# Performance work log

Measured on AMD Instinct MI355X. Metric: run time of the kernel, lower is better.

## Reference

```python
import jax, jax.numpy as jnp
import numpy as np
import math

BLK_NUM, BLK_SIZE = 128, 8
DIM, N_HEADS, N_KV_HEADS = 1024, 16, 4
HEAD_DIM = DIM // N_HEADS            # 64
HIDDEN = 64 * ((DIM + 63) // 64)     # 1024 (FeedForward hidden_dim)
BATCH = 4
SEQ = BLK_NUM * BLK_SIZE             # 1024
EPS = 1e-6
ROPE_THETA = 10000.0


def setup_inputs() -> dict:
    key = jax.random.key(0)
    ks = jax.random.split(key, 12)
    std = 1.0 / math.sqrt(DIM)
    f32 = jnp.float32
    inp = {
        "x":   jax.random.normal(ks[0], (BATCH, SEQ, DIM), f32),
        "vec": jax.random.normal(ks[1], (BATCH, BLK_NUM, DIM), f32),
        "wq": jax.random.normal(ks[2], (N_HEADS * HEAD_DIM, DIM), f32) * std,
        "wk": jax.random.normal(ks[3], (N_KV_HEADS * HEAD_DIM, DIM), f32) * std,
        "wv": jax.random.normal(ks[4], (N_KV_HEADS * HEAD_DIM, DIM), f32) * std,
        "wo": jax.random.normal(ks[5], (DIM, N_HEADS * HEAD_DIM), f32) * std,
        "w1": jax.random.normal(ks[6], (HIDDEN, DIM), f32) * std,
        "w2": jax.random.normal(ks[7], (DIM, HIDDEN), f32) * std,
        "w3": jax.random.normal(ks[8], (HIDDEN, DIM), f32) * std,
        "mod_attn_w": jax.random.normal(ks[9], (3 * DIM, DIM), f32) * std,
        "mod_attn_b": jnp.zeros((3 * DIM,), f32),
        "mod_ffn_w":  jax.random.normal(ks[10], (3 * DIM, DIM), f32) * std,
        "mod_ffn_b":  jnp.zeros((3 * DIM,), f32),
        "norm1_w": jnp.ones((DIM,), f32),
        "norm2_w": jnp.ones((DIM,), f32),
    }
    # rotary tables (equivalent to llama-style precompute_freqs_cis, theta=rope_scaling)
    inv_freq = 1.0 / (ROPE_THETA ** (jnp.arange(0, HEAD_DIM, 2, dtype=f32) / HEAD_DIM))
    angles = jnp.outer(jnp.arange(SEQ, dtype=f32), inv_freq)  # (SEQ, HEAD_DIM//2)
    inp["freqs_cos"] = jnp.cos(angles)
    inp["freqs_sin"] = jnp.sin(angles)
    return inp


def _rmsnorm(x, w):
    return x * jax.lax.rsqrt(jnp.mean(x * x, axis=-1, keepdims=True) + EPS) * w


def _rope(x, cos, sin):
    # x: (B, L, H, Dh); pairs are adjacent dims, matching view_as_complex on (..., Dh//2, 2)
    x1, x2 = x[..., 0::2], x[..., 1::2]
    c, s = cos[None, :, None, :], sin[None, :, None, :]
    return jnp.stack([x1 * c - x2 * s, x1 * s + x2 * c], axis=-1).reshape(x.shape)


def _modulate(vec, w, b):
    # adaLN: silu(vec) -> 3*dim, chunked into shift/scale/gate, one vector per block
    out = jax.nn.silu(vec) @ w.T + b
    shift, scale, gate = jnp.split(out, 3, axis=-1)
    rep = lambda t: jnp.repeat(t, BLK_SIZE, axis=1)  # (B, M, D) -> (B, L, D)
    return rep(shift), rep(scale), rep(gate)


def _block_attention(xn, freqs_cos, freqs_sin, wq, wk, wv, wo):
    B, L, _ = xn.shape
    q = (xn @ wq.T).reshape(B, L, N_HEADS, HEAD_DIM)
    k = (xn @ wk.T).reshape(B, L, N_KV_HEADS, HEAD_DIM)
    v = (xn @ wv.T).reshape(B, L, N_KV_HEADS, HEAD_DIM)
    q = _rope(q, freqs_cos, freqs_sin)
    k = _rope(k, freqs_cos, freqs_sin)
    g = N_HEADS // N_KV_HEADS  # GQA expansion (enable_gqa in flex_attention)
    k = jnp.repeat(k, g, axis=2)
    v = jnp.repeat(v, g, axis=2)
    q, k, v = (t.transpose(0, 2, 1, 3) for t in (q, k, v))  # (B, H, L, Dh)
    scores = jnp.einsum('bhqd,bhkd->bhqk', q, k) * (1.0 / math.sqrt(HEAD_DIM))
    blk = jnp.arange(L) // BLK_SIZE
    allow = blk[:, None] >= blk[None, :]  # block-causal: full attn within block, causal across blocks
    scores = jnp.where(allow, scores, jnp.asarray(-1e9, scores.dtype))
    probs = jax.nn.softmax(scores, axis=-1)
    out = jnp.einsum('bhqk,bhkd->bhqd', probs, v)
    out = out.transpose(0, 2, 1, 3).reshape(B, L, N_HEADS * HEAD_DIM)
    return out @ wo.T


def reference(x, vec, freqs_cos, freqs_sin, wq, wk, wv, wo, w1, w2, w3,
              mod_attn_w, mod_attn_b, mod_ffn_w, mod_ffn_b, norm1_w, norm2_w):
    sh_a, sc_a, gt_a = _modulate(vec, mod_attn_w, mod_attn_b)
    xn = _rmsnorm(x, norm1_w) * (1.0 + sc_a) + sh_a
    h = x + gt_a * _block_attention(xn, freqs_cos, freqs_sin, wq, wk, wv, wo)
    sh_f, sc_f, gt_f = _modulate(vec, mod_ffn_w, mod_ffn_b)
    hn = _rmsnorm(h, norm2_w) * (1.0 + sc_f) + sh_f
    ffn = (jax.nn.silu(hn @ w1.T) * (hn @ w3.T)) @ w2.T  # SwiGLU FeedForward
    return h + gt_f * ffn
```

## Files before the change

### kernel.cpp

```cpp
#include <hip/hip_runtime.h>
#include <math.h>

#define SEQ 1024
#define DIM 1024

using short8 = __attribute__((ext_vector_type(8))) short;
using f32x4  = __attribute__((ext_vector_type(4))) float;

__device__ __forceinline__ unsigned short f2bf(float f) {
  unsigned int u = __float_as_uint(f);
  u = (u + 0x7FFFu + ((u >> 16) & 1u)) >> 16;
  return (unsigned short)u;
}
__device__ __forceinline__ float bf2f(unsigned short h) {
  return __uint_as_float(((unsigned int)h) << 16);
}
__device__ __forceinline__ void load16_lds(const unsigned short* g, unsigned short* l) {
  __builtin_amdgcn_global_load_lds((const __attribute__((address_space(1))) void*)g,
                                   (__attribute__((address_space(3))) void*)l, 16, 0, 0);
}

struct CastArgs {
  const float* src[9];
  unsigned short* dst[9];
  int n[9];
};
__global__ __launch_bounds__(256) void cast_weights(CastArgs a) {
  int r = blockIdx.y;
  int i4 = (blockIdx.x * 256 + threadIdx.x) * 4;
  if (i4 >= a.n[r]) return;
  const float4 v = *(const float4*)(a.src[r] + i4);
  ushort4 o;
  o.x = f2bf(v.x); o.y = f2bf(v.y); o.z = f2bf(v.z); o.w = f2bf(v.w);
  *(ushort4*)(a.dst[r] + i4) = o;
}

__global__ __launch_bounds__(256) void silu_cast(const float* __restrict__ v,
                                                 unsigned short* __restrict__ o, int n) {
  int i4 = (blockIdx.x * 256 + threadIdx.x) * 4;
  if (i4 >= n) return;
  float4 x = *(const float4*)(v + i4);
  ushort4 r;
  r.x = f2bf(x.x / (1.0f + expf(-x.x)));
  r.y = f2bf(x.y / (1.0f + expf(-x.y)));
  r.z = f2bf(x.z / (1.0f + expf(-x.z)));
  r.w = f2bf(x.w / (1.0f + expf(-x.w)));
  *(ushort4*)(o + i4) = r;
}

template<int EPI>
__global__ __launch_bounds__(256) void mfma_gemm(
    const unsigned short* __restrict__ A, const unsigned short* __restrict__ W,
    int M, int N, int K,
    float* __restrict__ outF, unsigned short* __restrict__ outBF,
    const float* __restrict__ aux1,
    const float* __restrict__ aux2,
    const float* __restrict__ fc, const float* __restrict__ fs)
{
  __shared__ unsigned short sA[128 * 32];
  __shared__ unsigned short sB[64 * 32];
  const int tid = threadIdx.x;
  const int lane = tid & 63;
  const int wv = tid >> 6;
  const int wr = wv >> 1;
  const int wc = wv & 1;
  const int rowBlk = blockIdx.y * 128;
  const int colBlk = blockIdx.x * 64;
  const int l4 = lane >> 2;
  const int lk = (lane & 3) * 8;
  const int q = lane >> 4;
  const int cl = lane & 15;

  f32x4 acc[4][2] = {};

  for (int k0 = 0; k0 < K; k0 += 32) {
#pragma unroll
    for (int c = 0; c < 2; ++c) {
      int ch = wv * 2 + c;
      load16_lds(A + (size_t)(rowBlk + ch * 16 + l4) * K + k0 + lk, &sA[ch * 512 + lane * 8]);
    }
    load16_lds(W + (size_t)(colBlk + wv * 16 + l4) * K + k0 + lk, &sB[wv * 512 + lane * 8]);
    __syncthreads();
    short8 af[4], bfr[2];
#pragma unroll
    for (int t = 0; t < 4; ++t)
      af[t]  = *(const short8*)&sA[(wr * 64 + t * 16 + cl) * 32 + q * 8];
#pragma unroll
    for (int t = 0; t < 2; ++t)
      bfr[t] = *(const short8*)&sB[(wc * 32 + t * 16 + cl) * 32 + q * 8];
#pragma unroll
    for (int tm = 0; tm < 4; ++tm)
#pragma unroll
      for (int tn = 0; tn < 2; ++tn)
        acc[tm][tn] = __builtin_amdgcn_mfma_f32_16x16x32_bf16(af[tm], bfr[tn], acc[tm][tn], 0, 0, 0);
    __syncthreads();
  }

#pragma unroll
  for (int tm = 0; tm < 4; ++tm) {
#pragma unroll
    for (int tn = 0; tn < 2; ++tn) {
      const int col = colBlk + wc * 32 + tn * 16 + cl;
#pragma unroll
      for (int r = 0; r < 4; ++r) {
        const int row = rowBlk + wr * 64 + tm * 16 + q * 4 + r;
        float v = acc[tm][tn][r];
        if constexpr (EPI == 0) {
          float other = __shfl_xor(v, 1);
          if (col < 1280) {
            int s = row & (SEQ - 1);
            int t = (col & 63) >> 1;
            float cv = fc[s * 32 + t], sv = fs[s * 32 + t];
            v = ((col & 1) == 0) ? (v * cv - other * sv) : (other * sv + v * cv);
          }
          outBF[(size_t)row * N + col] = f2bf(v);
        } else if constexpr (EPI == 1) {
          float bb = (col < 3072) ? aux1[col] : aux2[col - 3072];
          outF[(size_t)row * N + col] = v + bb;
        } else if constexpr (EPI == 2 || EPI == 4) {
          int vr = (row >> 10) * 128 + ((row & (SEQ - 1)) >> 3);
          outF[(size_t)row * N + col] =
              aux1[(size_t)row * N + col] + aux2[(size_t)vr * 6144 + col] * v;
        } else if constexpr (EPI == 3) {
          outBF[(size_t)row * N + col] = f2bf(v);
        }
      }
    }
  }
}

__global__ __launch_bounds__(256) void rms_mod(
    const float* __restrict__ X, const float* __restrict__ w,
    const float* __restrict__ mod, int off, unsigned short* __restrict__ out)
{
  const int r = blockIdx.x;
  const int b = r >> 10, s = r & (SEQ - 1);
  const int vr = b * 128 + (s >> 3);
  const size_t base = (size_t)r * DIM;
  float v[4];
  float ss = 0.f;
#pragma unroll
  for (int p = 0; p < 4; ++p) {
    int c = threadIdx.x + p * 256;
    v[p] = X[base + c];
    ss += v[p] * v[p];
  }
#pragma unroll
  for (int o = 1; o < 64; o <<= 1) ss += __shfl_xor(ss, o);
  __shared__ float red[4];
  int lane = threadIdx.x & 63, wvv = threadIdx.x >> 6;
  if (lane == 0) red[wvv] = ss;
  __syncthreads();
  float total = red[0] + red[1] + red[2] + red[3];
  float rn = rsqrtf(total * (1.0f / 1024.0f) + 1e-6f);
  const float* mrow = mod + (size_t)vr * 6144 + off;
#pragma unroll
  for (int p = 0; p < 4; ++p) {
    int c = threadIdx.x + p * 256;
    out[base + c] = f2bf(v[p] * rn * w[c] * (1.0f + mrow[1024 + c]) + mrow[c]);
  }
}

__global__ __launch_bounds__(256) void attn_mfma(
    const unsigned short* __restrict__ QKV, unsigned short* __restrict__ O)
{
  const int bid = blockIdx.x;
  const int pr = bid & 7;
  const int h = (bid >> 3) & 15;
  const int b = bid >> 7;
  const int kvh = h >> 2;
  __shared__ unsigned short sK[64 * 64];
  __shared__ unsigned short sVt[64 * 72];
  __shared__ unsigned short sP[4][16 * 72];
  const int tid = threadIdx.x;
  const int lane = tid & 63;
  const int w = tid >> 6;
  const int q = lane >> 4;
  const int cl = lane & 15;
  const float SCL = 0.125f * 1.44269504f;

  for (int ph = 0; ph < 2; ++ph) {
    const int qt = ph ? (15 - pr) : pr;

    short8 qf[2];
    {
      const size_t qrow = (size_t)(b * SEQ + qt * 64 + w * 16 + cl) * 1536 + h * 64;
#pragma unroll
      for (int s = 0; s < 2; ++s)
        qf[s] = *(const short8*)(QKV + qrow + s * 32 + q * 8);
    }

    f32x4 accO[4] = {};
    float m_r[4], l_r[4];
#pragma unroll
    for (int r = 0; r < 4; ++r) { m_r[r] = -1e30f; l_r[r] = 0.f; }

    for (int kt = 0; kt <= qt; ++kt) {
      __syncthreads();
      {
        int rr = tid >> 3;
        int d0 = (tid & 7) * 8;
#pragma unroll
        for (int ppp = 0; ppp < 2; ++ppp) {
          int key = ppp * 32 + rr;
          const unsigned short* g =
              QKV + (size_t)(b * SEQ + kt * 64 + key) * 1536 + 1024 + kvh * 64 + d0;
          short8 kv = *(const short8*)g;
          *(short8*)(sK + key * 64 + (d0 ^ ((key & 7) * 8))) = kv;
        }
        int d = tid & 63;
        int kg = tid >> 6;
#pragma unroll
        for (int ppp = 0; ppp < 2; ++ppp) {
          int key0 = ppp * 32 + kg * 8;
          unsigned short tmp[8];
#pragma unroll
          for (int j = 0; j < 8; ++j)
            tmp[j] = QKV[(size_t)(b * SEQ + kt * 64 + key0 + j) * 1536 + 1280 + kvh * 64 + d];
          *(short8*)(sVt + d * 72 + key0) = *(const short8*)tmp;
        }
      }
      __syncthreads();

      f32x4 accS[4] = {};
#pragma unroll
      for (int s = 0; s < 2; ++s) {
#pragma unroll
        for (int n = 0; n < 4; ++n) {
          int rowk = n * 16 + cl;
          short8 kf = *(const short8*)(sK + rowk * 64 + ((s * 32 + q * 8) ^ ((cl & 7) * 8)));
          accS[n] = __builtin_amdgcn_mfma_f32_16x16x32_bf16(qf[s], kf, accS[n], 0, 0, 0);
        }
      }

      float sv[4][4];
      const bool diag = (kt == qt);
      const int qblk = w * 2 + (q >> 1);
#pragma unroll
      for (int n = 0; n < 4; ++n) {
        const bool msk = diag && (n * 2 + (cl >> 3)) > qblk;
#pragma unroll
        for (int r = 0; r < 4; ++r)
          sv[n][r] = msk ? -1e30f : accS[n][r] * SCL;
      }

      float alpha[4];
#pragma unroll
      for (int r = 0; r < 4; ++r) {
        float vmax = fmaxf(fmaxf(sv[0][r], sv[1][r]), fmaxf(sv[2][r], sv[3][r]));
        vmax = fmaxf(vmax, __shfl_xor(vmax, 1));
        vmax = fmaxf(vmax, __shfl_xor(vmax, 2));
        vmax = fmaxf(vmax, __shfl_xor(vmax, 4));
        vmax = fmaxf(vmax, __shfl_xor(vmax, 8));
        float mnew = fmaxf(m_r[r], vmax);
        alpha[r] = exp2f(m_r[r] - mnew);
        float rs = 0.f;
#pragma unroll
        for (int n = 0; n < 4; ++n) {
          float pp = exp2f(sv[n][r] - mnew);
          sv[n][r] = pp;
          rs += pp;
        }
        rs += __shfl_xor(rs, 1);
        rs += __shfl_xor(rs, 2);
        rs += __shfl_xor(rs, 4);
        rs += __shfl_xor(rs, 8);
        l_r[r] = l_r[r] * alpha[r] + rs;
        m_r[r] = mnew;
      }

#pragma unroll
      for (int n = 0; n < 4; ++n)
#pragma unroll
        for (int r = 0; r < 4; ++r)
          sP[w][(q * 4 + r) * 72 + n * 16 + cl] = f2bf(sv[n][r]);

#pragma unroll
      for (int dn = 0; dn < 4; ++dn) {
        accO[dn][0] *= alpha[0];
        accO[dn][1] *= alpha[1];
        accO[dn][2] *= alpha[2];
        accO[dn][3] *= alpha[3];
      }

      short8 pf[2];
      pf[0] = *(const short8*)(&sP[w][cl * 72 + q * 8]);
      pf[1] = *(const short8*)(&sP[w][cl * 72 + 32 + q * 8]);
#pragma unroll
      for (int dn = 0; dn < 4; ++dn) {
#pragma unroll
        for (int s = 0; s < 2; ++s) {
          short8 vf = *(const short8*)(sVt + (dn * 16 + cl) * 72 + s * 32 + q * 8);
          accO[dn] = __builtin_amdgcn_mfma_f32_16x16x32_bf16(pf[s], vf, accO[dn], 0, 0, 0);
        }
      }
    }

    float invl[4];
#pragma unroll
    for (int r = 0; r < 4; ++r) invl[r] = 1.0f / l_r[r];
#pragma unroll
    for (int dn = 0; dn < 4; ++dn)
#pragma unroll
      for (int r = 0; r < 4; ++r) {
        int row = b * SEQ + qt * 64 + w * 16 + q * 4 + r;
        O[(size_t)row * DIM + h * 64 + dn * 16 + cl] = f2bf(accO[dn][r] * invl[r]);
      }
    __syncthreads();
  }
}

__global__ __launch_bounds__(256) void swiglu(const unsigned short* __restrict__ U,
                                              unsigned short* __restrict__ G)
{
  int gid = blockIdx.x * 256 + threadIdx.x;
  int row = gid >> 7;
  int col = (gid & 127) * 8;
  short8 u1 = *(const short8*)(U + (size_t)row * 2048 + col);
  short8 u3 = *(const short8*)(U + (size_t)row * 2048 + 1024 + col);
  short8 g;
#pragma unroll
  for (int j = 0; j < 8; ++j) {
    float f1 = bf2f((unsigned short)u1[j]);
    float f3 = bf2f((unsigned short)u3[j]);
    float s = f1 / (1.0f + expf(-f1)) * f3;
    g[j] = (short)f2bf(s);
  }
  *(short8*)(G + (size_t)row * 1024 + col) = g;
}

extern "C" void kernel_launch(void* const* d_in, const int* in_sizes, int n_in,
                              void* d_out, int out_size, void* d_ws, size_t ws_size,
                              hipStream_t stream)
{
  const float* x   = (const float*)d_in[0];
  const float* vec = (const float*)d_in[1];
  const float* wq  = (const float*)d_in[2];
  const float* wk  = (const float*)d_in[3];
  const float* wv  = (const float*)d_in[4];
  const float* wo  = (const float*)d_in[5];
  const float* w1  = (const float*)d_in[6];
  const float* w2  = (const float*)d_in[7];
  const float* w3  = (const float*)d_in[8];
  const float* maw = (const float*)d_in[9];
  const float* mab = (const float*)d_in[10];
  const float* mfw = (const float*)d_in[11];
  const float* mfb = (const float*)d_in[12];
  const float* n1w = (const float*)d_in[13];
  const float* n2w = (const float*)d_in[14];
  const float* fc  = (const float*)d_in[15];
  const float* fs  = (const float*)d_in[16];

  char* p = (char*)d_ws;
  auto takeU = [&](size_t elems) { unsigned short* r = (unsigned short*)p; p += elems * 2; return r; };
  auto takeF = [&](size_t elems) { float* r = (float*)p; p += elems * 4; return r; };

  unsigned short* WQKV = takeU((size_t)1536 * 1024);
  unsigned short* WOb  = takeU((size_t)1024 * 1024);
  unsigned short* W13  = takeU((size_t)2048 * 1024);
  unsigned short* W2b  = takeU((size_t)1024 * 1024);
  unsigned short* WM   = takeU((size_t)6144 * 1024);
  unsigned short* SVEC = takeU((size_t)512 * 1024);
  float* MOD  = takeF((size_t)512 * 6144);
  float* H    = takeF((size_t)4096 * 1024);
  unsigned short* XNb  = takeU((size_t)4096 * 1024);
  unsigned short* QKVb = takeU((size_t)4096 * 1536);
  unsigned short* AOb  = takeU((size_t)4096 * 1024);
  unsigned short* HNb  = takeU((size_t)4096 * 1024);
  unsigned short* U13 = XNb;
  unsigned short* Gb  = AOb;

  dim3 blk(256);

  CastArgs ca;
  ca.src[0] = wq;  ca.dst[0] = WQKV;                    ca.n[0] = 1024 * 1024;
  ca.src[1] = wk;  ca.dst[1] = WQKV + 1024 * 1024;      ca.n[1] = 256 * 1024;
  ca.src[2] = wv;  ca.dst[2] = WQKV + 1280 * 1024;      ca.n[2] = 256 * 1024;
  ca.src[3] = wo;  ca.dst[3] = WOb;                     ca.n[3] = 1024 * 1024;
  ca.src[4] = w1;  ca.dst[4] = W13;                     ca.n[4] = 1024 * 1024;
  ca.src[5] = w3;  ca.dst[5] = W13 + 1024 * 1024;       ca.n[5] = 1024 * 1024;
  ca.src[6] = w2;  ca.dst[6] = W2b;                     ca.n[6] = 1024 * 1024;
  ca.src[7] = maw; ca.dst[7] = WM;                      ca.n[7] = 3072 * 1024;
  ca.src[8] = mfw; ca.dst[8] = WM + (size_t)3072 * 1024; ca.n[8] = 3072 * 1024;
  cast_weights<<<dim3(3072, 9), blk, 0, stream>>>(ca);

  silu_cast<<<512, blk, 0, stream>>>(vec, SVEC, 512 * 1024);

  mfma_gemm<1><<<dim3(96, 4), blk, 0, stream>>>(SVEC, WM, 512, 6144, 1024,
      MOD, nullptr, mab, mfb, nullptr, nullptr);

  rms_mod<<<4096, blk, 0, stream>>>(x, n1w, MOD, 0, XNb);

  mfma_gemm<0><<<dim3(24, 32), blk, 0, stream>>>(XNb, WQKV, 4096, 1536, 1024,
      nullptr, QKVb, nullptr, nullptr, fc, fs);

  attn_mfma<<<512, blk, 0, stream>>>(QKVb, AOb);

  mfma_gemm<2><<<dim3(16, 32), blk, 0, stream>>>(AOb, WOb, 4096, 1024, 1024,
      H, nullptr, x, MOD + 2048, nullptr, nullptr);

  rms_mod<<<4096, blk, 0, stream>>>(H, n2w, MOD, 3072, HNb);

  mfma_gemm<3><<<dim3(32, 32), blk, 0, stream>>>(HNb, W13, 4096, 2048, 1024,
      nullptr, U13, nullptr, nullptr, nullptr, nullptr);

  swiglu<<<2048, blk, 0, stream>>>(U13, Gb);

  mfma_gemm<4><<<dim3(16, 32), blk, 0, stream>>>(Gb, W2b, 4096, 1024, 1024,
      (float*)d_out, nullptr, H, MOD + 5120, nullptr, nullptr);
}
```

Before: 338.8 us.

## Double-buffer GEMM LDS with BK=64 swizzle and fuse SwiGLU into W13 epilogue

The GEMM K-tile grows from 32 to 64, and the LDS tiles are double-buffered with an XOR swizzle, so the next tile's global-to-LDS loads overlap the MFMA work and one barrier is dropped per iteration. The w1 and w3 weights are row-interleaved during the cast, so each output column pair holds matching gate and up values. The W13 GEMM epilogue then applies SwiGLU through a lane shuffle and writes the gated result directly, which removes the separate swiglu kernel and the intermediate U13 buffer. LDS use per block grows fourfold, which may reduce occupancy.

New measurement: 326.7 us. 1.04x faster.

```diff
diff --git a/kernel.cpp b/kernel.cpp
--- a/kernel.cpp
+++ b/kernel.cpp
@@ -24,6 +24,7 @@
   const float* src[9];
   unsigned short* dst[9];
   int n[9];
+  int ilv[9];
 };
 __global__ __launch_bounds__(256) void cast_weights(CastArgs a) {
   int r = blockIdx.y;
@@ -32,7 +33,9 @@
   const float4 v = *(const float4*)(a.src[r] + i4);
   ushort4 o;
   o.x = f2bf(v.x); o.y = f2bf(v.y); o.z = f2bf(v.z); o.w = f2bf(v.w);
-  *(ushort4*)(a.dst[r] + i4) = o;
+  size_t di = i4;
+  if (a.ilv[r]) di = (size_t)((i4 >> 10) * 2 + (a.ilv[r] - 1)) * 1024 + (i4 & 1023);
+  *(ushort4*)(a.dst[r] + di) = o;
 }
 
 __global__ __launch_bounds__(256) void silu_cast(const float* __restrict__ v,
@@ -57,8 +60,8 @@
     const float* __restrict__ aux2,
     const float* __restrict__ fc, const float* __restrict__ fs)
 {
-  __shared__ unsigned short sA[128 * 32];
-  __shared__ unsigned short sB[64 * 32];
+  __shared__ unsigned short sA[2][128 * 64];
+  __shared__ unsigned short sB[2][64 * 64];
   const int tid = threadIdx.x;
   const int lane = tid & 63;
   const int wv = tid >> 6;
@@ -66,35 +69,63 @@
   const int wc = wv & 1;
   const int rowBlk = blockIdx.y * 128;
   const int colBlk = blockIdx.x * 64;
-  const int l4 = lane >> 2;
-  const int lk = (lane & 3) * 8;
   const int q = lane >> 4;
   const int cl = lane & 15;
 
   f32x4 acc[4][2] = {};
 
-  for (int k0 = 0; k0 < K; k0 += 32) {
-#pragma unroll
-    for (int c = 0; c < 2; ++c) {
-      int ch = wv * 2 + c;
-      load16_lds(A + (size_t)(rowBlk + ch * 16 + l4) * K + k0 + lk, &sA[ch * 512 + lane * 8]);
-    }
-    load16_lds(W + (size_t)(colBlk + wv * 16 + l4) * K + k0 + lk, &sB[wv * 512 + lane * 8]);
+  auto stage = [&](int bf, int k0) {
+#pragma unroll
+    for (int j = 0; j < 4; ++j) {
+      int slot = j * 256 + tid;
+      int row = slot >> 3;
+      int cg = (slot & 7) ^ (row & 7);
+      load16_lds(A + (size_t)(rowBlk + row) * K + k0 + cg * 8, &sA[bf][slot * 8]);
+    }
+#pragma unroll
+    for (int j = 0; j < 2; ++j) {
+      int slot = j * 256 + tid;
+      int row = slot >> 3;
+      int cg = (slot & 7) ^ (row & 7);
+      load16_lds(W + (size_t)(colBlk + row) * K + k0 + cg * 8, &sB[bf][slot * 8]);
+    }
+  };
+
+  auto compute = [&](int bf) {
+    short8 af[4][2], bfr[2][2];
+#pragma unroll
+    for (int t = 0; t < 4; ++t) {
+      int row = wr * 64 + t * 16 + cl;
+#pragma unroll
+      for (int s = 0; s < 2; ++s)
+        af[t][s] = *(const short8*)&sA[bf][row * 64 + (((s * 4 + q) ^ (cl & 7)) * 8)];
+    }
+#pragma unroll
+    for (int t = 0; t < 2; ++t) {
+      int row = wc * 32 + t * 16 + cl;
+#pragma unroll
+      for (int s = 0; s < 2; ++s)
+        bfr[t][s] = *(const short8*)&sB[bf][row * 64 + (((s * 4 + q) ^ (cl & 7)) * 8)];
+    }
+#pragma unroll
+    for (int s = 0; s < 2; ++s)
+#pragma unroll
+      for (int tm = 0; tm < 4; ++tm)
+#pragma unroll
+        for (int tn = 0; tn < 2; ++tn)
+          acc[tm][tn] = __builtin_amdgcn_mfma_f32_16x16x32_bf16(af[tm][s], bfr[tn][s], acc[tm][tn], 0, 0, 0);
+  };
+
+  stage(0, 0);
+  int cur = 0;
+  for (int k0 = 64; k0 < K; k0 += 64) {
     __syncthreads();
-    short8 af[4], bfr[2];
-#pragma unroll
-    for (int t = 0; t < 4; ++t)
-      af[t]  = *(const short8*)&sA[(wr * 64 + t * 16 + cl) * 32 + q * 8];
-#pragma unroll
-    for (int t = 0; t < 2; ++t)
-      bfr[t] = *(const short8*)&sB[(wc * 32 + t * 16 + cl) * 32 + q * 8];
-#pragma unroll
-    for (int tm = 0; tm < 4; ++tm)
-#pragma unroll
-      for (int tn = 0; tn < 2; ++tn)
-        acc[tm][tn] = __builtin_amdgcn_mfma_f32_16x16x32_bf16(af[tm], bfr[tn], acc[tm][tn], 0, 0, 0);
-    __syncthreads();
+    stage(cur ^ 1, k0);
+    compute(cur);
+    cur ^= 1;
   }
+  __syncthreads();
+  compute(cur);
 
 #pragma unroll
   for (int tm = 0; tm < 4; ++tm) {
@@ -122,7 +153,11 @@
           outF[(size_t)row * N + col] =
               aux1[(size_t)row * N + col] + aux2[(size_t)vr * 6144 + col] * v;
         } else if constexpr (EPI == 3) {
-          outBF[(size_t)row * N + col] = f2bf(v);
+          float other = __shfl_xor(v, 1);
+          if ((col & 1) == 0) {
+            float g = v / (1.0f + expf(-v)) * other;
+            outBF[(size_t)row * 1024 + (col >> 1)] = f2bf(g);
+          }
         }
       }
     }
@@ -308,25 +343,6 @@
       }
     __syncthreads();
   }
-}
-
-__global__ __launch_bounds__(256) void swiglu(const unsigned short* __restrict__ U,
-                                              unsigned short* __restrict__ G)
-{
-  int gid = blockIdx.x * 256 + threadIdx.x;
-  int row = gid >> 7;
-  int col = (gid & 127) * 8;
-  short8 u1 = *(const short8*)(U + (size_t)row * 2048 + col);
-  short8 u3 = *(const short8*)(U + (size_t)row * 2048 + 1024 + col);
-  short8 g;
-#pragma unroll
-  for (int j = 0; j < 8; ++j) {
-    float f1 = bf2f((unsigned short)u1[j]);
-    float f3 = bf2f((unsigned short)u3[j]);
-    float s = f1 / (1.0f + expf(-f1)) * f3;
-    g[j] = (short)f2bf(s);
-  }
-  *(short8*)(G + (size_t)row * 1024 + col) = g;
 }
 
 extern "C" void kernel_launch(void* const* d_in, const int* in_sizes, int n_in,
@@ -367,21 +383,20 @@
   unsigned short* QKVb = takeU((size_t)4096 * 1536);
   unsigned short* AOb  = takeU((size_t)4096 * 1024);
   unsigned short* HNb  = takeU((size_t)4096 * 1024);
-  unsigned short* U13 = XNb;
   unsigned short* Gb  = AOb;
 
   dim3 blk(256);
 
   CastArgs ca;
-  ca.src[0] = wq;  ca.dst[0] = WQKV;                    ca.n[0] = 1024 * 1024;
-  ca.src[1] = wk;  ca.dst[1] = WQKV + 1024 * 1024;      ca.n[1] = 256 * 1024;
-  ca.src[2] = wv;  ca.dst[2] = WQKV + 1280 * 1024;      ca.n[2] = 256 * 1024;
-  ca.src[3] = wo;  ca.dst[3] = WOb;                     ca.n[3] = 1024 * 1024;
-  ca.src[4] = w1;  ca.dst[4] = W13;                     ca.n[4] = 1024 * 1024;
-  ca.src[5] = w3;  ca.dst[5] = W13 + 1024 * 1024;       ca.n[5] = 1024 * 1024;
-  ca.src[6] = w2;  ca.dst[6] = W2b;                     ca.n[6] = 1024 * 1024;
-  ca.src[7] = maw; ca.dst[7] = WM;                      ca.n[7] = 3072 * 1024;
-  ca.src[8] = mfw; ca.dst[8] = WM + (size_t)3072 * 1024; ca.n[8] = 3072 * 1024;
+  ca.src[0] = wq;  ca.dst[0] = WQKV;                    ca.n[0] = 1024 * 1024; ca.ilv[0] = 0;
+  ca.src[1] = wk;  ca.dst[1] = WQKV + 1024 * 1024;      ca.n[1] = 256 * 1024;  ca.ilv[1] = 0;
+  ca.src[2] = wv;  ca.dst[2] = WQKV + 1280 * 1024;      ca.n[2] = 256 * 1024;  ca.ilv[2] = 0;
+  ca.src[3] = wo;  ca.dst[3] = WOb;                     ca.n[3] = 1024 * 1024; ca.ilv[3] = 0;
+  ca.src[4] = w1;  ca.dst[4] = W13;                     ca.n[4] = 1024 * 1024; ca.ilv[4] = 1;
+  ca.src[5] = w3;  ca.dst[5] = W13;                     ca.n[5] = 1024 * 1024; ca.ilv[5] = 2;
+  ca.src[6] = w2;  ca.dst[6] = W2b;                     ca.n[6] = 1024 * 1024; ca.ilv[6] = 0;
+  ca.src[7] = maw; ca.dst[7] = WM;                      ca.n[7] = 3072 * 1024; ca.ilv[7] = 0;
+  ca.src[8] = mfw; ca.dst[8] = WM + (size_t)3072 * 1024; ca.n[8] = 3072 * 1024; ca.ilv[8] = 0;
   cast_weights<<<dim3(3072, 9), blk, 0, stream>>>(ca);
 
   silu_cast<<<512, blk, 0, stream>>>(vec, SVEC, 512 * 1024);
@@ -402,9 +417,7 @@
   rms_mod<<<4096, blk, 0, stream>>>(H, n2w, MOD, 3072, HNb);
 
   mfma_gemm<3><<<dim3(32, 32), blk, 0, stream>>>(HNb, W13, 4096, 2048, 1024,
-      nullptr, U13, nullptr, nullptr, nullptr, nullptr);
-
-  swiglu<<<2048, blk, 0, stream>>>(U13, Gb);
+      nullptr, Gb, nullptr, nullptr, nullptr, nullptr);
 
   mfma_gemm<4><<<dim3(16, 32), blk, 0, stream>>>(Gb, W2b, 4096, 1024, 1024,
       (float*)d_out, nullptr, H, MOD + 5120, nullptr, nullptr);
```
